# Kernel optimization log

Measured on AMD Instinct MI355X. Metric: run time of the kernel, lower is better.

## Reference

```python
import jax, jax.numpy as jnp
import numpy as np

RADIUS = 96
B, IN, OUT, DYN, K = 32, 32, 32, 16, 7


def hex_neighbor_indices(radius):
    # Hex grid cells in axial coords: |i|<r, |k|<r, |i-k|<r, lexicographic order.
    cells = [(i, k) for i in range(-radius + 1, radius)
             for k in range(-radius + 1, radius) if abs(i - k) < radius]
    idx = {c: n for n, c in enumerate(cells)}
    offsets = [(-1, -1), (-1, 0), (0, -1), (0, 0), (0, 1), (1, 0), (1, 1)]
    nbr = np.full((len(offsets), len(cells)), -1, np.int32)
    for n, (i, k) in enumerate(cells):
        for o, (di, dk) in enumerate(offsets):
            nbr[o, n] = idx.get((i + di, k + dk), -1)
    return nbr


def setup_inputs() -> dict:
    key = jax.random.key(0)
    k1, k2, k3, k4 = jax.random.split(key, 4)
    nbr = hex_neighbor_indices(RADIUS)          # (7, N), -1 = invalid neighbor
    N = nbr.shape[1]                            # 3r^2-3r+1 = 27361
    return {
        "grid": jax.random.normal(k1, (B, N, IN), jnp.float32),
        "dyn": jax.random.normal(k2, (B, K, DYN), jnp.float32),
        "neighbor_idx": jnp.asarray(nbr),
        "Wdyn": jax.random.normal(k3, (K, DYN, IN, OUT), jnp.float32) * 0.05,
        "Wstatic": jax.random.normal(k4, (K, IN, OUT), jnp.float32) * 0.05,
        "bias": jnp.zeros((OUT,), jnp.float32),
    }


def reference(grid, dyn, neighbor_idx, Wdyn, Wstatic, bias):
    # grid: (B, N, in), dyn: (B, 7, dyn_dim), neighbor_idx: (7, N)
    mask = neighbor_idx >= 0                      # (7, N)
    safe = jnp.where(mask, neighbor_idx, 0)
    gathered = jnp.take(grid, safe, axis=1)       # (B, 7, N, in)
    gathered = gathered * mask[None, :, :, None].astype(grid.dtype)
    # dynamic per-neighbor kernel: einsum('bd,dio->bio') for each k
    dyn_kernel = jnp.einsum('bkd,kdio->bkio', dyn, Wdyn)      # (B, 7, in, out)
    dyn_proj = jnp.einsum('bkni,bkio->bno', gathered, dyn_kernel)
    static_proj = jnp.einsum('bkni,kio->bno', gathered, Wstatic)
    return dyn_proj + static_proj + bias          # (B, N, out); shrink=False, no activation
```

## Files before the change

kernel.cpp:

```cpp
#include <hip/hip_runtime.h>
#include <hip/hip_bf16.h>

typedef __attribute__((ext_vector_type(8))) short short8;
typedef __attribute__((ext_vector_type(4))) float f32x4;

static constexpr int IN = 32, OUT = 32, DYNDIM = 16, KNBR = 7;
static constexpr int ROWS = 512;
static constexpr int PAD  = 192;
static constexpr int WIN  = ROWS + 2 * PAD;
static constexpr int LROW = 36;
static constexpr int NT   = 512;

__device__ inline unsigned short f2bf(float f) {
    unsigned u = __builtin_bit_cast(unsigned, f);
    unsigned r = (u + 0x7fffu + ((u >> 16) & 1u)) >> 16;
    return (unsigned short)r;
}

__global__ void pack_weights(const float* __restrict__ dyn,
                             const float* __restrict__ Wdyn,
                             const float* __restrict__ Wstat,
                             unsigned short* __restrict__ Wp)
{
    int bk = blockIdx.x;
    int k  = bk % KNBR;
    __shared__ float dsh[DYNDIM];
    if (threadIdx.x < DYNDIM)
        dsh[threadIdx.x] = dyn[(size_t)bk * DYNDIM + threadIdx.x];
    __syncthreads();

    for (int e = threadIdx.x; e < IN * OUT; e += blockDim.x) {
        int i = e >> 5, o = e & 31;
        float acc = Wstat[((size_t)k * IN + i) * OUT + o];
        const float* wd = Wdyn + (((size_t)k * DYNDIM) * IN + i) * OUT + o;
#pragma unroll
        for (int d = 0; d < DYNDIM; ++d)
            acc += dsh[d] * wd[(size_t)d * IN * OUT];
        int ch = o >> 4, cc = o & 15, g = i >> 3, j = i & 7;
        Wp[(((size_t)bk * 2 + ch) * 64 + (g * 16 + cc)) * 8 + j] = f2bf(acc);
    }
}

__global__ __launch_bounds__(NT, 2) void hexconv_fused(
    const float* __restrict__ grid,
    const int* __restrict__ nbr,
    const unsigned short* __restrict__ Wp,
    const float* __restrict__ bias,
    float* __restrict__ out,
    int N)
{
    __shared__ unsigned short wlds[KNBR * 1024];
    __shared__ unsigned short glds[WIN * LROW];

    const int b      = blockIdx.y;
    const int base   = blockIdx.x * ROWS;
    const int win_lo = base - PAD;
    const size_t gbase = (size_t)b * N * 32;

    const unsigned short* wpb = Wp + (size_t)b * KNBR * 1024;
    for (int e = threadIdx.x; e < KNBR * 128; e += NT)
        *(short8*)(wlds + (size_t)e * 8) = *(const short8*)(wpb + (size_t)e * 8);

    for (int e = threadIdx.x; e < WIN * 4; e += NT) {
        int row = e >> 2, seg = e & 3;
        int gr = win_lo + row;
        if (gr >= 0 && gr < N) {
            const float* gp = grid + gbase + (size_t)gr * 32 + seg * 8;
            float4 x0 = *(const float4*)gp;
            float4 x1 = *(const float4*)(gp + 4);
            short8 v;
            v[0] = (short)f2bf(x0.x); v[1] = (short)f2bf(x0.y);
            v[2] = (short)f2bf(x0.z); v[3] = (short)f2bf(x0.w);
            v[4] = (short)f2bf(x1.x); v[5] = (short)f2bf(x1.y);
            v[6] = (short)f2bf(x1.z); v[7] = (short)f2bf(x1.w);
            *(short8*)(glds + row * LROW + seg * 8) = v;
        }
    }
    __syncthreads();

    const int lane = threadIdx.x & 63;
    const int w    = threadIdx.x >> 6;
    const int g    = lane >> 4;
    const int c    = lane & 15;
    const int wbase = base + w * 64;
    const float bc0 = bias[c];
    const float bc1 = bias[16 + c];

#pragma unroll
    for (int t = 0; t < 4; ++t) {
        const int n0 = wbase + t * 16 + c;
        const bool valid = (n0 < N);
        int idxv[KNBR];
#pragma unroll
        for (int kk = 0; kk < KNBR; ++kk) {
            if (kk == 3) idxv[kk] = valid ? n0 : -1;
            else         idxv[kk] = valid ? nbr[(size_t)kk * N + n0] : -1;
        }

        f32x4 acc0 = {0.f, 0.f, 0.f, 0.f};
        f32x4 acc1 = {0.f, 0.f, 0.f, 0.f};
#pragma unroll
        for (int kk = 0; kk < KNBR; ++kk) {
            short8 a = {0, 0, 0, 0, 0, 0, 0, 0};
            int id = idxv[kk];
            if (id >= 0)
                a = *(const short8*)(glds + (size_t)(id - win_lo) * LROW + g * 8);
            short8 b0 = *(const short8*)(wlds + kk * 1024 + lane * 8);
            short8 b1 = *(const short8*)(wlds + kk * 1024 + 512 + lane * 8);
            acc0 = __builtin_amdgcn_mfma_f32_16x16x32_bf16(a, b0, acc0, 0, 0, 0);
            acc1 = __builtin_amdgcn_mfma_f32_16x16x32_bf16(a, b1, acc1, 0, 0, 0);
        }

        const int row_base = wbase + t * 16 + g * 4;
#pragma unroll
        for (int r = 0; r < 4; ++r) {
            int row = row_base + r;
            if (row < N) {
                float* op = out + gbase + (size_t)row * 32;
                op[c]      = acc0[r] + bc0;
                op[16 + c] = acc1[r] + bc1;
            }
        }
    }
}

extern "C" void kernel_launch(void* const* d_in, const int* in_sizes, int n_in,
                              void* d_out, int out_size, void* d_ws, size_t ws_size,
                              hipStream_t stream)
{
    const float* grid  = (const float*)d_in[0];
    const float* dyn   = (const float*)d_in[1];
    const int*   nbr   = (const int*)d_in[2];
    const float* Wdyn  = (const float*)d_in[3];
    const float* Wstat = (const float*)d_in[4];
    const float* bias  = (const float*)d_in[5];
    float* out = (float*)d_out;

    const int N = in_sizes[2] / KNBR;
    const int B = in_sizes[0] / (N * IN);

    unsigned short* Wp = (unsigned short*)d_ws;
    pack_weights<<<B * KNBR, 256, 0, stream>>>(dyn, Wdyn, Wstat, Wp);

    dim3 grd((N + ROWS - 1) / ROWS, B);
    hexconv_fused<<<grd, NT, 0, stream>>>(grid, nbr, Wp, bias, out, N);
}
```

Before: 66.93 us.

## Keep per-batch weights in registers, prefetch neighbor indices, remap workgroups across XCDs

```diff
diff --git a/kernel.cpp b/kernel.cpp
--- a/kernel.cpp
+++ b/kernel.cpp
@@ -41,7 +41,7 @@
     }
 }
 
-__global__ __launch_bounds__(NT, 2) void hexconv_fused(
+__global__ __launch_bounds__(NT, 4) void hexconv_fused(
     const float* __restrict__ grid,
     const int* __restrict__ nbr,
     const unsigned short* __restrict__ Wp,
@@ -49,17 +49,47 @@
     float* __restrict__ out,
     int N)
 {
-    __shared__ unsigned short wlds[KNBR * 1024];
     __shared__ unsigned short glds[WIN * LROW];
 
-    const int b      = blockIdx.y;
-    const int base   = blockIdx.x * ROWS;
+    const int nwgx = gridDim.x;
+    const int nwg  = nwgx * gridDim.y;
+    int orig = blockIdx.x + nwgx * blockIdx.y;
+    int wg = orig;
+    if ((nwg & 7) == 0) {
+        int cpx = nwg >> 3;
+        wg = (orig & 7) * cpx + (orig >> 3);
+    }
+    const int bx = wg % nwgx;
+    const int b  = wg / nwgx;
+
+    const int base   = bx * ROWS;
     const int win_lo = base - PAD;
     const size_t gbase = (size_t)b * N * 32;
 
+    const int lane = threadIdx.x & 63;
+    const int w    = threadIdx.x >> 6;
+    const int g    = lane >> 4;
+    const int c    = lane & 15;
+    const int wbase = base + w * 64;
+
     const unsigned short* wpb = Wp + (size_t)b * KNBR * 1024;
-    for (int e = threadIdx.x; e < KNBR * 128; e += NT)
-        *(short8*)(wlds + (size_t)e * 8) = *(const short8*)(wpb + (size_t)e * 8);
+    short8 bw[KNBR][2];
+#pragma unroll
+    for (int kk = 0; kk < KNBR; ++kk)
+#pragma unroll
+        for (int ch = 0; ch < 2; ++ch)
+            bw[kk][ch] = *(const short8*)(wpb + ((size_t)(kk * 2 + ch) * 64 + lane) * 8);
+
+    int idxc[KNBR];
+    {
+        const int n0 = wbase + c;
+        const bool v = (n0 < N);
+#pragma unroll
+        for (int kk = 0; kk < KNBR; ++kk) {
+            if (kk == 3) idxc[kk] = v ? n0 : -1;
+            else         idxc[kk] = v ? nbr[(size_t)kk * N + n0] : -1;
+        }
+    }
 
     for (int e = threadIdx.x; e < WIN * 4; e += NT) {
         int row = e >> 2, seg = e & 3;
@@ -68,33 +98,30 @@
             const float* gp = grid + gbase + (size_t)gr * 32 + seg * 8;
             float4 x0 = *(const float4*)gp;
             float4 x1 = *(const float4*)(gp + 4);
-            short8 v;
-            v[0] = (short)f2bf(x0.x); v[1] = (short)f2bf(x0.y);
-            v[2] = (short)f2bf(x0.z); v[3] = (short)f2bf(x0.w);
-            v[4] = (short)f2bf(x1.x); v[5] = (short)f2bf(x1.y);
-            v[6] = (short)f2bf(x1.z); v[7] = (short)f2bf(x1.w);
-            *(short8*)(glds + row * LROW + seg * 8) = v;
+            short8 vv;
+            vv[0] = (short)f2bf(x0.x); vv[1] = (short)f2bf(x0.y);
+            vv[2] = (short)f2bf(x0.z); vv[3] = (short)f2bf(x0.w);
+            vv[4] = (short)f2bf(x1.x); vv[5] = (short)f2bf(x1.y);
+            vv[6] = (short)f2bf(x1.z); vv[7] = (short)f2bf(x1.w);
+            *(short8*)(glds + row * LROW + seg * 8) = vv;
         }
     }
     __syncthreads();
 
-    const int lane = threadIdx.x & 63;
-    const int w    = threadIdx.x >> 6;
-    const int g    = lane >> 4;
-    const int c    = lane & 15;
-    const int wbase = base + w * 64;
     const float bc0 = bias[c];
     const float bc1 = bias[16 + c];
 
 #pragma unroll
     for (int t = 0; t < 4; ++t) {
-        const int n0 = wbase + t * 16 + c;
-        const bool valid = (n0 < N);
-        int idxv[KNBR];
+        int idxn[KNBR];
+        if (t < 3) {
+            const int n1 = wbase + (t + 1) * 16 + c;
+            const bool v = (n1 < N);
 #pragma unroll
-        for (int kk = 0; kk < KNBR; ++kk) {
-            if (kk == 3) idxv[kk] = valid ? n0 : -1;
-            else         idxv[kk] = valid ? nbr[(size_t)kk * N + n0] : -1;
+            for (int kk = 0; kk < KNBR; ++kk) {
+                if (kk == 3) idxn[kk] = v ? n1 : -1;
+                else         idxn[kk] = v ? nbr[(size_t)kk * N + n1] : -1;
+            }
         }
 
         f32x4 acc0 = {0.f, 0.f, 0.f, 0.f};
@@ -102,13 +129,11 @@
 #pragma unroll
         for (int kk = 0; kk < KNBR; ++kk) {
             short8 a = {0, 0, 0, 0, 0, 0, 0, 0};
-            int id = idxv[kk];
+            int id = idxc[kk];
             if (id >= 0)
                 a = *(const short8*)(glds + (size_t)(id - win_lo) * LROW + g * 8);
-            short8 b0 = *(const short8*)(wlds + kk * 1024 + lane * 8);
-            short8 b1 = *(const short8*)(wlds + kk * 1024 + 512 + lane * 8);
-            acc0 = __builtin_amdgcn_mfma_f32_16x16x32_bf16(a, b0, acc0, 0, 0, 0);
-            acc1 = __builtin_amdgcn_mfma_f32_16x16x32_bf16(a, b1, acc1, 0, 0, 0);
+            acc0 = __builtin_amdgcn_mfma_f32_16x16x32_bf16(a, bw[kk][0], acc0, 0, 0, 0);
+            acc1 = __builtin_amdgcn_mfma_f32_16x16x32_bf16(a, bw[kk][1], acc1, 0, 0, 0);
         }
 
         const int row_base = wbase + t * 16 + g * 4;
@@ -120,6 +145,11 @@
                 op[c]      = acc0[r] + bc0;
                 op[16 + c] = acc1[r] + bc1;
             }
+        }
+
+        if (t < 3) {
+#pragma unroll
+            for (int kk = 0; kk < KNBR; ++kk) idxc[kk] = idxn[kk];
         }
     }
 }
```

Result: faster. 57.08 us (-14.7%).
